# Optimization experiments

Hardware: AMD Instinct MI355X
Metric: run time of the kernel (lower is better)

Reference implementation:

```python
import jax, jax.numpy as jnp
import numpy as np

LEAKY_SLOPE = 0.01  # torch nn.LeakyReLU default

def _mlp(x, w1, b1, w2, b2):
    # MLP_Layer(num_layers=2, batch_norm=False): Linear -> ReLU -> Linear
    return jax.nn.relu(x @ w1 + b1) @ w2 + b2

def _edge_softmax(scores, dst, num_nodes):
    # softmax over incoming edges of each destination node; scores: [E, H]
    m = jax.ops.segment_max(scores, dst, num_segments=num_nodes)  # [N, H]
    e = jnp.exp(scores - m[dst])
    s = jax.ops.segment_sum(e, dst, num_segments=num_nodes)       # [N, H]
    return e / s[dst]

def setup_inputs() -> dict:
    key = jax.random.key(0)
    ks = jax.random.split(key, 10)
    N, E, H = 50000, 800000, 4
    D_H, PCA, PI, HID = 64, 64, 32, 128
    inp = {
        "h":    jax.random.normal(ks[0], (N, D_H), jnp.float32),
        "pca":  jax.random.normal(ks[1], (N, PCA), jnp.float32),
        "pimg": jax.random.normal(ks[2], (N, PI), jnp.float32),
        "pca_w1": jax.random.normal(ks[3], (2 * PCA, HID), jnp.float32) * (1.0 / np.sqrt(2 * PCA)),
        "pca_b1": jnp.zeros((HID,), jnp.float32),
        "pca_w2": jax.random.normal(ks[4], (HID, H), jnp.float32) * (1.0 / np.sqrt(HID)),
        "pca_b2": jnp.zeros((H,), jnp.float32),
        "pi_w1": jax.random.normal(ks[5], (2 * PI, HID), jnp.float32) * (1.0 / np.sqrt(2 * PI)),
        "pi_b1": jnp.zeros((HID,), jnp.float32),
        "pi_w2": jax.random.normal(ks[6], (HID, H), jnp.float32) * (1.0 / np.sqrt(HID)),
        "pi_b2": jnp.zeros((H,), jnp.float32),
        "src": jax.random.randint(ks[7], (E,), 0, N, jnp.int32),
        "dst": jax.random.randint(ks[8], (E,), 0, N, jnp.int32),
    }
    return inp

def reference(h, pca, pimg, pca_w1, pca_b1, pca_w2, pca_b2,
              pi_w1, pi_b1, pi_w2, pi_b2, src, dst):
    N = h.shape[0]

    def attend(feat, w1, b1, w2, b2):
        e_feat = jnp.concatenate([feat[src], feat[dst]], axis=1)        # [E, 2F]
        score = jax.nn.leaky_relu(_mlp(e_feat, w1, b1, w2, b2), LEAKY_SLOPE)  # [E, H]
        a = _edge_softmax(score, dst, N)                                # [E, H]
        msg = h[src][:, None, :] * a[:, :, None]                        # [E, H, D]
        return jax.ops.segment_sum(msg, dst, num_segments=N)           # [N, H, D]

    out_pca = attend(pca, pca_w1, pca_b1, pca_w2, pca_b2)
    out_pi = attend(pimg, pi_w1, pi_b1, pi_w2, pi_b2)
    return jnp.concatenate([out_pca, out_pi], axis=-1)                  # [N, H, 2D]
```

## Files before the change

kernel.cpp:

```cpp
#include <hip/hip_runtime.h>
#include <hip/hip_fp16.h>

constexpr int HID = 128;
constexpr int DH  = 64;

typedef _Float16 f16x2 __attribute__((ext_vector_type(2)));
typedef _Float16 fh4   __attribute__((ext_vector_type(4)));
typedef _Float16 fh8   __attribute__((ext_vector_type(8)));
typedef float    f32x4v __attribute__((ext_vector_type(4)));

__device__ __forceinline__ fh8 relu8(fh8 x) {
  fh8 z = {0, 0, 0, 0, 0, 0, 0, 0};
#if __has_builtin(__builtin_elementwise_max)
  return __builtin_elementwise_max(x, z);
#else
  fh8 r;
#pragma unroll
  for (int i = 0; i < 8; i++) r[i] = x[i] > z[i] ? x[i] : z[i];
  return r;
#endif
}

__global__ void count_h16_kernel(const int* __restrict__ dst, int* __restrict__ counts, int E,
                                 const float* __restrict__ h, _Float16* __restrict__ h16, int total) {
  int i = blockIdx.x * 256 + threadIdx.x;
  if (i < E) atomicAdd(&counts[dst[i]], 1);
  int base = i * 8;
  if (base + 7 < total) {
    float4 f0 = *(const float4*)(h + base);
    float4 f1 = *(const float4*)(h + base + 4);
    fh8 t;
    t[0] = (_Float16)f0.x; t[1] = (_Float16)f0.y; t[2] = (_Float16)f0.z; t[3] = (_Float16)f0.w;
    t[4] = (_Float16)f1.x; t[5] = (_Float16)f1.y; t[6] = (_Float16)f1.z; t[7] = (_Float16)f1.w;
    *(fh8*)(h16 + base) = t;
  }
}

__launch_bounds__(256)
__global__ void uv_mfma_kernel(const float* __restrict__ pca, const float* __restrict__ pimg,
                               const float* __restrict__ b1a, const float* __restrict__ b1b,
                               const float* __restrict__ w1a, const float* __restrict__ w1b,
                               _Float16* __restrict__ u_cat, _Float16* __restrict__ v_cat, int N) {
  __shared__ _Float16 sB[16384];
  int rel = blockIdx.y;
  const float* feat = rel ? pimg : pca;
  const float* b1   = rel ? b1b : b1a;
  const float* w1   = rel ? w1b : w1a;
  int F  = rel ? 32 : 64;
  int KS = rel ? 1 : 2;
  int tid = threadIdx.x;
  for (int idx = tid; idx < 16384; idx += 256) {
    int g = idx >> 10, s = (idx >> 9) & 1, l = (idx >> 3) & 63, j = idx & 7;
    int bc = l & 15, bkg = l >> 4;
    int k = s * 32 + bkg * 8 + j;
    float val = 0.f;
    if (k < F) {
      int jslot = (g & 7) * 16 + bc;
      int krow = (g < 8) ? k : (F + k);
      val = w1[krow * HID + jslot];
    }
    sB[idx] = (_Float16)val;
  }
  __syncthreads();
  int lane = tid & 63, w = tid >> 6;
  int c = lane & 15, kg = lane >> 4;
  int node = blockIdx.x * 64 + w * 16 + c;
  int nclamp = node < N ? node : N - 1;
  fh8 bfeat[2];
#pragma unroll
  for (int s = 0; s < 2; s++) {
    if (s < KS) {
      const float* fp = feat + (size_t)nclamp * F + s * 32 + kg * 8;
      float4 f0 = *(const float4*)fp;
      float4 f1 = *(const float4*)(fp + 4);
      fh8 t;
      t[0] = (_Float16)f0.x; t[1] = (_Float16)f0.y; t[2] = (_Float16)f0.z; t[3] = (_Float16)f0.w;
      t[4] = (_Float16)f1.x; t[5] = (_Float16)f1.y; t[6] = (_Float16)f1.z; t[7] = (_Float16)f1.w;
      bfeat[s] = t;
    }
  }
  float4 b1q[8];
#pragma unroll
  for (int g = 0; g < 8; g++) b1q[g] = *(const float4*)(b1 + g * 16 + kg * 4);

  bool wr = node < N;
#pragma unroll
  for (int g = 0; g < 16; g++) {
    f32x4v acc = {0.f, 0.f, 0.f, 0.f};
    acc = __builtin_amdgcn_mfma_f32_16x16x32_f16(((const fh8*)sB)[(g * 2 + 0) * 64 + lane], bfeat[0], acc, 0, 0, 0);
    if (KS == 2)
      acc = __builtin_amdgcn_mfma_f32_16x16x32_f16(((const fh8*)sB)[(g * 2 + 1) * 64 + lane], bfeat[1], acc, 0, 0, 0);
    bool isv = g >= 8;
    int jbase = (g & 7) * 16 + kg * 4;
    float4 bias = isv ? b1q[g & 7] : make_float4(0.f, 0.f, 0.f, 0.f);
    fh4 pk;
    pk[0] = (_Float16)(acc[0] + bias.x);
    pk[1] = (_Float16)(acc[1] + bias.y);
    pk[2] = (_Float16)(acc[2] + bias.z);
    pk[3] = (_Float16)(acc[3] + bias.w);
    _Float16* outp = isv ? v_cat : u_cat;
    if (wr) *(fh4*)(outp + (size_t)node * 256 + rel * 128 + jbase) = pk;
  }
}

__launch_bounds__(256)
__global__ void scan1_kernel(const int* __restrict__ counts, int* __restrict__ bsums, int N) {
  int b = blockIdx.x, tid = threadIdx.x;
  int base = b * 1024 + tid * 4;
  int s = 0;
  if (base + 3 < N) {
    int4 v = *(const int4*)(counts + base);
    s = v.x + v.y + v.z + v.w;
  } else {
    for (int q = 0; q < 4; q++) { int idx = base + q; if (idx < N) s += counts[idx]; }
  }
#pragma unroll
  for (int o = 32; o >= 1; o >>= 1) s += __shfl_xor(s, o);
  __shared__ int ws[4];
  if ((tid & 63) == 0) ws[tid >> 6] = s;
  __syncthreads();
  if (tid == 0) bsums[b] = ws[0] + ws[1] + ws[2] + ws[3];
}

__launch_bounds__(256)
__global__ void scan23_kernel(const int* __restrict__ counts, const int* __restrict__ bsums,
                              int* __restrict__ offsets, int* __restrict__ cursor,
                              int NB, int N, int E) {
  int b = blockIdx.x, tid = threadIdx.x, lane = tid & 63, w = tid >> 6;
  __shared__ int s_bpre;
  if (tid < 64) {
    int v = (lane < NB) ? bsums[lane] : 0;
    int incl = v;
#pragma unroll
    for (int o = 1; o < 64; o <<= 1) { int t = __shfl_up(incl, o); if (lane >= o) incl += t; }
    int excl = incl - v;
    int t = __shfl(excl, b);
    if (lane == 0) s_bpre = t;
  }
  __syncthreads();
  int base = b * 1024 + tid * 4;
  int c[4] = {0, 0, 0, 0};
  if (base + 3 < N) {
    int4 v = *(const int4*)(counts + base);
    c[0] = v.x; c[1] = v.y; c[2] = v.z; c[3] = v.w;
  } else {
    for (int q = 0; q < 4; q++) { int idx = base + q; if (idx < N) c[q] = counts[idx]; }
  }
  int s = c[0] + c[1] + c[2] + c[3];
  int incl = s;
#pragma unroll
  for (int o = 1; o < 64; o <<= 1) { int t = __shfl_up(incl, o); if (lane >= o) incl += t; }
  int excl = incl - s;
  __shared__ int ws[4];
  if (lane == 63) ws[w] = incl;
  __syncthreads();
  int wpre = 0;
  for (int q = 0; q < w; q++) wpre += ws[q];
  int off = s_bpre + wpre + excl;
  for (int q = 0; q < 4; q++) {
    int idx = base + q;
    if (idx < N) { offsets[idx] = off; cursor[idx] = off; }
    off += c[q];
  }
  if (b == 0 && tid == 0) offsets[N] = E;
}

__global__ void fill_kernel(const int* __restrict__ src, const int* __restrict__ dst,
                            int* __restrict__ cursor, int2* __restrict__ edges, int E) {
  int e = blockIdx.x * 256 + threadIdx.x;
  if (e < E) {
    int d = dst[e];
    int pos = atomicAdd(&cursor[d], 1);
    edges[pos] = make_int2(src[e], d);
  }
}

__launch_bounds__(256, 8)
__global__ void score_kernel(const _Float16* __restrict__ u_cat, const _Float16* __restrict__ v_cat,
                             const int2* __restrict__ edges,
                             const float* __restrict__ w2a, const float* __restrict__ w2b,
                             const float* __restrict__ b2a, const float* __restrict__ b2b,
                             _Float16* __restrict__ ek, int E) {
  __shared__ _Float16 sB[8 * 64 * 8];
  int tid = threadIdx.x, lane = tid & 63, w = tid >> 6;
  int col = lane & 15, kg = lane >> 4;
  for (int idx = tid; idx < 4096; idx += 256) {
    int t = idx >> 9, l = (idx >> 3) & 63, j = idx & 7;
    int bc = l & 15;
    int k = t * 32 + ((l >> 4) << 3) + j;
    float val = 0.f;
    if (bc < 4) { if (k < 128) val = w2a[k * 4 + bc]; }
    else if (bc < 8) { if (k >= 128) val = w2b[(k - 128) * 4 + (bc - 4)]; }
    sB[idx] = (_Float16)val;
  }
  __syncthreads();

  int ebase = blockIdx.x * 256 + w * 64;
  const _Float16* up[4];
  const _Float16* vp[4];
#pragma unroll
  for (int m = 0; m < 4; m++) {
    int em = ebase + m * 16 + col;
    int ec = em < E ? em : 0;
    int2 sd = edges[ec];
    up[m] = u_cat + (size_t)sd.x * 256 + kg * 8;
    vp[m] = v_cat + (size_t)sd.y * 256 + kg * 8;
  }

  f32x4v acc[4];
#pragma unroll
  for (int m = 0; m < 4; m++) acc[m] = (f32x4v){0.f, 0.f, 0.f, 0.f};

#pragma unroll
  for (int t = 0; t < 8; t++) {
    fh8 bf = *(const fh8*)(sB + ((t * 64 + lane) << 3));
#pragma unroll
    for (int m = 0; m < 4; m++) {
      fh8 uu = *(const fh8*)(up[m] + t * 32);
      fh8 vv = *(const fh8*)(vp[m] + t * 32);
      acc[m] = __builtin_amdgcn_mfma_f32_16x16x32_f16(relu8(uu + vv), bf, acc[m], 0, 0, 0);
    }
  }

  if (col < 8) {
    float b2v = (col < 4) ? b2a[col] : b2b[col - 4];
#pragma unroll
    for (int m = 0; m < 4; m++) {
#pragma unroll
      for (int q = 0; q < 4; q++) {
        int er = ebase + m * 16 + kg * 4 + q;
        if (er < E) {
          float x = acc[m][q] + b2v;
          x = x > 0.f ? x : 0.01f * x;
          ek[(size_t)er * 8 + col] = (_Float16)__expf(x);
        }
      }
    }
  }
}

__launch_bounds__(256, 8)
__global__ void agg_kernel(const _Float16* __restrict__ ek, const int2* __restrict__ edges,
                           const int* __restrict__ offsets, const _Float16* __restrict__ h16,
                           float* __restrict__ out, int N) {
  int wid = blockIdx.x * 4 + (threadIdx.x >> 6);
  int lane = threadIdx.x & 63;
  if (wid >= N) return;
  int off0 = offsets[wid], off1 = offsets[wid + 1];
  int deg = off1 - off0;
  float* op = out + (size_t)wid * 512;
  if (deg == 0) {
#pragma unroll
    for (int k = 0; k < 4; k++) { op[k * 128 + lane] = 0.f; op[k * 128 + 64 + lane] = 0.f; }
    return;
  }
  float accO[8] = {0, 0, 0, 0, 0, 0, 0, 0};
  float ssum[8] = {0, 0, 0, 0, 0, 0, 0, 0};
  int last = off1 - 1;
  int s0 = edges[off0].x;
  int s1 = edges[min(off0 + 1, last)].x;
  int s2 = edges[min(off0 + 2, last)].x;
  int s3 = edges[min(off0 + 3, last)].x;
  for (int jj = 0; jj < deg; jj += 4) {
    int i0 = off0 + jj;
    int i1 = min(i0 + 1, last), i2 = min(i0 + 2, last), i3 = min(i0 + 3, last);
    bool m1 = jj + 1 < deg, m2 = jj + 2 < deg, m3 = jj + 3 < deg;
    fh8 e0 = *(const fh8*)(ek + (size_t)i0 * 8);
    fh8 e1 = *(const fh8*)(ek + (size_t)i1 * 8);
    fh8 e2 = *(const fh8*)(ek + (size_t)i2 * 8);
    fh8 e3 = *(const fh8*)(ek + (size_t)i3 * 8);
    float hv0 = (float)h16[(size_t)s0 * DH + lane];
    float hv1 = (float)h16[(size_t)s1 * DH + lane];
    float hv2 = (float)h16[(size_t)s2 * DH + lane];
    float hv3 = (float)h16[(size_t)s3 * DH + lane];
    int t0 = edges[min(i0 + 4, last)].x;
    int t1 = edges[min(i0 + 5, last)].x;
    int t2 = edges[min(i0 + 6, last)].x;
    int t3 = edges[min(i0 + 7, last)].x;
#pragma unroll
    for (int k = 0; k < 8; k++) {
      float e0v = (float)e0[k];
      float e1v = m1 ? (float)e1[k] : 0.f;
      float e2v = m2 ? (float)e2[k] : 0.f;
      float e3v = m3 ? (float)e3[k] : 0.f;
      accO[k] = fmaf(e0v, hv0, accO[k]);
      accO[k] = fmaf(e1v, hv1, accO[k]);
      accO[k] = fmaf(e2v, hv2, accO[k]);
      accO[k] = fmaf(e3v, hv3, accO[k]);
      ssum[k] += (e0v + e1v) + (e2v + e3v);
    }
    s0 = t0; s1 = t1; s2 = t2; s3 = t3;
  }
#pragma unroll
  for (int k = 0; k < 8; k++) {
    float rsv = 1.f / ssum[k];
    int colo = k < 4 ? k * 128 + lane : (k - 4) * 128 + 64 + lane;
    op[colo] = accO[k] * rsv;
  }
}

extern "C" void kernel_launch(void* const* d_in, const int* in_sizes, int n_in,
                              void* d_out, int out_size, void* d_ws, size_t ws_size,
                              hipStream_t stream) {
  const float* h      = (const float*)d_in[0];
  const float* pca    = (const float*)d_in[1];
  const float* pimg   = (const float*)d_in[2];
  const float* pca_w1 = (const float*)d_in[3];
  const float* pca_b1 = (const float*)d_in[4];
  const float* pca_w2 = (const float*)d_in[5];
  const float* pca_b2 = (const float*)d_in[6];
  const float* pi_w1  = (const float*)d_in[7];
  const float* pi_b1  = (const float*)d_in[8];
  const float* pi_w2  = (const float*)d_in[9];
  const float* pi_b2  = (const float*)d_in[10];
  const int*   src    = (const int*)d_in[11];
  const int*   dst    = (const int*)d_in[12];
  int N = in_sizes[0] / 64;
  int E = in_sizes[11];
  float* out = (float*)d_out;

  char* ws = (char*)d_ws;
  size_t o = 0;
  auto alloc = [&](size_t bytes) { void* p = ws + o; o += (bytes + 255) & ~(size_t)255; return p; };
  _Float16* u_cat  = (_Float16*)alloc((size_t)N * 256 * 2);
  _Float16* v_cat  = (_Float16*)alloc((size_t)N * 256 * 2);
  _Float16* h16    = (_Float16*)alloc((size_t)N * 64 * 2);
  int* counts  = (int*)alloc((size_t)N * 4);
  int* cursor  = (int*)alloc((size_t)N * 4);
  int* offsets = (int*)alloc((size_t)(N + 1) * 4);
  int* bsums   = (int*)alloc(1024 * 4);
  int2* edges  = (int2*)alloc((size_t)E * 8);
  _Float16* ekb = (_Float16*)alloc((size_t)E * 8 * 2);

  hipMemsetAsync(counts, 0, (size_t)N * 4, stream);

  count_h16_kernel<<<(E + 255) / 256, 256, 0, stream>>>(dst, counts, E, h, h16, N * 64);
  dim3 uvgrid((N + 63) / 64, 2);
  uv_mfma_kernel<<<uvgrid, 256, 0, stream>>>(pca, pimg, pca_b1, pi_b1, pca_w1, pi_w1, u_cat, v_cat, N);
  int NB = (N + 1023) / 1024;
  scan1_kernel<<<NB, 256, 0, stream>>>(counts, bsums, N);
  scan23_kernel<<<NB, 256, 0, stream>>>(counts, bsums, offsets, cursor, NB, N, E);
  fill_kernel<<<(E + 255) / 256, 256, 0, stream>>>(src, dst, cursor, edges, E);
  score_kernel<<<(E + 255) / 256, 256, 0, stream>>>(u_cat, v_cat, edges,
                                                    pca_w2, pi_w2, pca_b2, pi_b2, ekb, E);
  agg_kernel<<<(N + 3) / 4, 256, 0, stream>>>(ekb, edges, offsets, h16, out, N);
}
```

Before: 304.8 us.

## Fuse edge scoring with CSR aggregation and precompute W1 fragment table once

The separate score and aggregation kernels are merged. Each wave takes a 64-edge chunk of the dst-sorted edge list, finds its node range by binary search over the offsets, computes the exp scores with MFMA into shared memory, and then accumulates h-weighted messages per destination node, writing each output row when it reaches a node boundary. This removes the round trip of the E×8 fp16 score buffer through global memory and one kernel launch. The W1 fragment layout is also built once into a global table by the count kernel, so the uv blocks copy it instead of rebuilding it from scattered fp32 loads. In exchange, the aggregation loop now runs serially per edge with no unrolling, occupancy is lowered to 6 blocks, and waves do uneven work because of binary search and boundary handling.

```diff
diff --git a/kernel.cpp b/kernel.cpp
--- a/kernel.cpp
+++ b/kernel.cpp
@@ -21,9 +21,28 @@
 #endif
 }
 
-__global__ void count_h16_kernel(const int* __restrict__ dst, int* __restrict__ counts, int E,
-                                 const float* __restrict__ h, _Float16* __restrict__ h16, int total) {
+__global__ void count_h16_frag_kernel(const int* __restrict__ dst, int* __restrict__ counts, int E,
+                                      const float* __restrict__ h, _Float16* __restrict__ h16, int total,
+                                      const float* __restrict__ w1a, const float* __restrict__ w1b,
+                                      _Float16* __restrict__ fragTab) {
   int i = blockIdx.x * 256 + threadIdx.x;
+  if (blockIdx.x < 128) {
+    int flat = i;
+    int rel = flat >> 14;
+    int r2 = flat & 16383;
+    int g = r2 >> 10, s = (r2 >> 9) & 1, l = (r2 >> 3) & 63, j = r2 & 7;
+    int bc = l & 15, bkg = l >> 4;
+    int k = s * 32 + bkg * 8 + j;
+    int F = rel ? 32 : 64;
+    const float* w1 = rel ? w1b : w1a;
+    float val = 0.f;
+    if (k < F) {
+      int jslot = (g & 7) * 16 + bc;
+      int krow = (g < 8) ? k : (F + k);
+      val = w1[krow * HID + jslot];
+    }
+    fragTab[flat] = (_Float16)val;
+  }
   if (i < E) atomicAdd(&counts[dst[i]], 1);
   int base = i * 8;
   if (base + 7 < total) {
@@ -39,27 +58,19 @@
 __launch_bounds__(256)
 __global__ void uv_mfma_kernel(const float* __restrict__ pca, const float* __restrict__ pimg,
                                const float* __restrict__ b1a, const float* __restrict__ b1b,
-                               const float* __restrict__ w1a, const float* __restrict__ w1b,
+                               const _Float16* __restrict__ fragTab,
                                _Float16* __restrict__ u_cat, _Float16* __restrict__ v_cat, int N) {
   __shared__ _Float16 sB[16384];
   int rel = blockIdx.y;
   const float* feat = rel ? pimg : pca;
   const float* b1   = rel ? b1b : b1a;
-  const float* w1   = rel ? w1b : w1a;
   int F  = rel ? 32 : 64;
   int KS = rel ? 1 : 2;
   int tid = threadIdx.x;
-  for (int idx = tid; idx < 16384; idx += 256) {
-    int g = idx >> 10, s = (idx >> 9) & 1, l = (idx >> 3) & 63, j = idx & 7;
-    int bc = l & 15, bkg = l >> 4;
-    int k = s * 32 + bkg * 8 + j;
-    float val = 0.f;
-    if (k < F) {
-      int jslot = (g & 7) * 16 + bc;
-      int krow = (g < 8) ? k : (F + k);
-      val = w1[krow * HID + jslot];
-    }
-    sB[idx] = (_Float16)val;
+  {
+    const fh8* srcp = (const fh8*)(fragTab + rel * 16384);
+    fh8* dstp = (fh8*)sB;
+    for (int i = tid; i < 2048; i += 256) dstp[i] = srcp[i];
   }
   __syncthreads();
   int lane = tid & 63, w = tid >> 6;
@@ -175,14 +186,17 @@
   }
 }
 
-__launch_bounds__(256, 8)
-__global__ void score_kernel(const _Float16* __restrict__ u_cat, const _Float16* __restrict__ v_cat,
-                             const int2* __restrict__ edges,
+__launch_bounds__(256, 6)
+__global__ void fused_kernel(const _Float16* __restrict__ u_cat, const _Float16* __restrict__ v_cat,
+                             const int2* __restrict__ edges, const int* __restrict__ offsets,
+                             const _Float16* __restrict__ h16,
                              const float* __restrict__ w2a, const float* __restrict__ w2b,
                              const float* __restrict__ b2a, const float* __restrict__ b2b,
-                             _Float16* __restrict__ ek, int E) {
-  __shared__ _Float16 sB[8 * 64 * 8];
-  int tid = threadIdx.x, lane = tid & 63, w = tid >> 6;
+                             float* __restrict__ out, int N, int NW) {
+  __shared__ _Float16 sB[4096];
+  __shared__ __align__(16) _Float16 s_ek[4][64][8];
+  __shared__ int s_src[4][64];
+  int tid = threadIdx.x, lane = tid & 63, wv = tid >> 6;
   int col = lane & 15, kg = lane >> 4;
   for (int idx = tid; idx < 4096; idx += 256) {
     int t = idx >> 9, l = (idx >> 3) & 63, j = idx & 7;
@@ -195,107 +209,121 @@
   }
   __syncthreads();
 
-  int ebase = blockIdx.x * 256 + w * 64;
-  const _Float16* up[4];
-  const _Float16* vp[4];
-#pragma unroll
-  for (int m = 0; m < 4; m++) {
-    int em = ebase + m * 16 + col;
-    int ec = em < E ? em : 0;
-    int2 sd = edges[ec];
-    up[m] = u_cat + (size_t)sd.x * 256 + kg * 8;
-    vp[m] = v_cat + (size_t)sd.y * 256 + kg * 8;
-  }
-
-  f32x4v acc[4];
-#pragma unroll
-  for (int m = 0; m < 4; m++) acc[m] = (f32x4v){0.f, 0.f, 0.f, 0.f};
-
-#pragma unroll
-  for (int t = 0; t < 8; t++) {
-    fh8 bf = *(const fh8*)(sB + ((t * 64 + lane) << 3));
+  int w = blockIdx.x * 4 + wv;
+  if (w >= NW) return;
+  int t0 = w * 64, t1 = t0 + 64;
+  int lo = 0, hi = N;
+  while (lo < hi) { int mid = (lo + hi) >> 1; if (offsets[mid] < t0) lo = mid + 1; else hi = mid; }
+  int nlo = lo;
+  hi = N;
+  while (lo < hi) { int mid = (lo + hi) >> 1; if (offsets[mid] < t1) lo = mid + 1; else hi = mid; }
+  int nhi = lo;
+  if (nlo >= nhi) return;
+  int e_begin = offsets[nlo], e_end = offsets[nhi];
+
+  float b2v = (col < 4) ? b2a[col] : ((col < 8) ? b2b[col - 4] : 0.f);
+
+  int cur = nlo;
+  int node_start = e_begin;
+  int boundary = offsets[cur + 1];
+  float accO[8] = {0, 0, 0, 0, 0, 0, 0, 0};
+  float ssum[8] = {0, 0, 0, 0, 0, 0, 0, 0};
+
+  for (int cb = e_begin; cb < e_end; cb += 64) {
+    __builtin_amdgcn_wave_barrier();
+    const _Float16* up[4];
+    const _Float16* vp[4];
+    int srcs[4];
 #pragma unroll
     for (int m = 0; m < 4; m++) {
-      fh8 uu = *(const fh8*)(up[m] + t * 32);
-      fh8 vv = *(const fh8*)(vp[m] + t * 32);
-      acc[m] = __builtin_amdgcn_mfma_f32_16x16x32_f16(relu8(uu + vv), bf, acc[m], 0, 0, 0);
-    }
-  }
-
-  if (col < 8) {
-    float b2v = (col < 4) ? b2a[col] : b2b[col - 4];
-#pragma unroll
-    for (int m = 0; m < 4; m++) {
-#pragma unroll
-      for (int q = 0; q < 4; q++) {
-        int er = ebase + m * 16 + kg * 4 + q;
-        if (er < E) {
+      int em = cb + m * 16 + col;
+      int ec = em < e_end ? em : e_end - 1;
+      int2 sd = edges[ec];
+      srcs[m] = sd.x;
+      up[m] = u_cat + (size_t)sd.x * 256 + kg * 8;
+      vp[m] = v_cat + (size_t)sd.y * 256 + kg * 8;
+    }
+    f32x4v acc[4];
+#pragma unroll
+    for (int m = 0; m < 4; m++) acc[m] = (f32x4v){0.f, 0.f, 0.f, 0.f};
+#pragma unroll
+    for (int t = 0; t < 8; t++) {
+      fh8 bf = *(const fh8*)(sB + ((t * 64 + lane) << 3));
+#pragma unroll
+      for (int m = 0; m < 4; m++) {
+        fh8 uu = *(const fh8*)(up[m] + t * 32);
+        fh8 vv = *(const fh8*)(vp[m] + t * 32);
+        acc[m] = __builtin_amdgcn_mfma_f32_16x16x32_f16(relu8(uu + vv), bf, acc[m], 0, 0, 0);
+      }
+    }
+    if (kg == 0) {
+#pragma unroll
+      for (int m = 0; m < 4; m++) s_src[wv][m * 16 + col] = srcs[m];
+    }
+    if (col < 8) {
+#pragma unroll
+      for (int m = 0; m < 4; m++) {
+#pragma unroll
+        for (int q = 0; q < 4; q++) {
           float x = acc[m][q] + b2v;
           x = x > 0.f ? x : 0.01f * x;
-          ek[(size_t)er * 8 + col] = (_Float16)__expf(x);
+          s_ek[wv][m * 16 + kg * 4 + q][col] = (_Float16)__expf(x);
         }
       }
     }
-  }
-}
-
-__launch_bounds__(256, 8)
-__global__ void agg_kernel(const _Float16* __restrict__ ek, const int2* __restrict__ edges,
-                           const int* __restrict__ offsets, const _Float16* __restrict__ h16,
-                           float* __restrict__ out, int N) {
-  int wid = blockIdx.x * 4 + (threadIdx.x >> 6);
-  int lane = threadIdx.x & 63;
-  if (wid >= N) return;
-  int off0 = offsets[wid], off1 = offsets[wid + 1];
-  int deg = off1 - off0;
-  float* op = out + (size_t)wid * 512;
-  if (deg == 0) {
-#pragma unroll
-    for (int k = 0; k < 4; k++) { op[k * 128 + lane] = 0.f; op[k * 128 + 64 + lane] = 0.f; }
-    return;
-  }
-  float accO[8] = {0, 0, 0, 0, 0, 0, 0, 0};
-  float ssum[8] = {0, 0, 0, 0, 0, 0, 0, 0};
-  int last = off1 - 1;
-  int s0 = edges[off0].x;
-  int s1 = edges[min(off0 + 1, last)].x;
-  int s2 = edges[min(off0 + 2, last)].x;
-  int s3 = edges[min(off0 + 3, last)].x;
-  for (int jj = 0; jj < deg; jj += 4) {
-    int i0 = off0 + jj;
-    int i1 = min(i0 + 1, last), i2 = min(i0 + 2, last), i3 = min(i0 + 3, last);
-    bool m1 = jj + 1 < deg, m2 = jj + 2 < deg, m3 = jj + 3 < deg;
-    fh8 e0 = *(const fh8*)(ek + (size_t)i0 * 8);
-    fh8 e1 = *(const fh8*)(ek + (size_t)i1 * 8);
-    fh8 e2 = *(const fh8*)(ek + (size_t)i2 * 8);
-    fh8 e3 = *(const fh8*)(ek + (size_t)i3 * 8);
-    float hv0 = (float)h16[(size_t)s0 * DH + lane];
-    float hv1 = (float)h16[(size_t)s1 * DH + lane];
-    float hv2 = (float)h16[(size_t)s2 * DH + lane];
-    float hv3 = (float)h16[(size_t)s3 * DH + lane];
-    int t0 = edges[min(i0 + 4, last)].x;
-    int t1 = edges[min(i0 + 5, last)].x;
-    int t2 = edges[min(i0 + 6, last)].x;
-    int t3 = edges[min(i0 + 7, last)].x;
-#pragma unroll
-    for (int k = 0; k < 8; k++) {
-      float e0v = (float)e0[k];
-      float e1v = m1 ? (float)e1[k] : 0.f;
-      float e2v = m2 ? (float)e2[k] : 0.f;
-      float e3v = m3 ? (float)e3[k] : 0.f;
-      accO[k] = fmaf(e0v, hv0, accO[k]);
-      accO[k] = fmaf(e1v, hv1, accO[k]);
-      accO[k] = fmaf(e2v, hv2, accO[k]);
-      accO[k] = fmaf(e3v, hv3, accO[k]);
-      ssum[k] += (e0v + e1v) + (e2v + e3v);
-    }
-    s0 = t0; s1 = t1; s2 = t2; s3 = t3;
-  }
-#pragma unroll
-  for (int k = 0; k < 8; k++) {
-    float rsv = 1.f / ssum[k];
-    int colo = k < 4 ? k * 128 + lane : (k - 4) * 128 + 64 + lane;
-    op[colo] = accO[k] * rsv;
+    __builtin_amdgcn_wave_barrier();
+    asm volatile("s_waitcnt lgkmcnt(0)" ::: "memory");
+    int cnt = min(64, e_end - cb);
+    for (int jj = 0; jj < cnt; jj++) {
+      int e = cb + jj;
+      while (e == boundary) {
+        int deg = boundary - node_start;
+        float* op = out + (size_t)cur * 512;
+        if (deg == 0) {
+#pragma unroll
+          for (int k = 0; k < 4; k++) { op[k * 128 + lane] = 0.f; op[k * 128 + 64 + lane] = 0.f; }
+        } else {
+#pragma unroll
+          for (int k = 0; k < 8; k++) {
+            float rsv = 1.f / ssum[k];
+            int colo = k < 4 ? k * 128 + lane : (k - 4) * 128 + 64 + lane;
+            op[colo] = accO[k] * rsv;
+          }
+        }
+#pragma unroll
+        for (int k = 0; k < 8; k++) { accO[k] = 0.f; ssum[k] = 0.f; }
+        node_start = boundary; cur++;
+        boundary = offsets[cur + 1];
+      }
+      fh8 ea = *(const fh8*)(&s_ek[wv][jj][0]);
+      int sa = s_src[wv][jj];
+      float hv = (float)h16[(size_t)sa * DH + lane];
+#pragma unroll
+      for (int k = 0; k < 8; k++) {
+        float ev = (float)ea[k];
+        accO[k] = fmaf(ev, hv, accO[k]);
+        ssum[k] += ev;
+      }
+    }
+  }
+  while (cur < nhi) {
+    int bnd = offsets[cur + 1];
+    int deg = bnd - node_start;
+    float* op = out + (size_t)cur * 512;
+    if (deg == 0) {
+#pragma unroll
+      for (int k = 0; k < 4; k++) { op[k * 128 + lane] = 0.f; op[k * 128 + 64 + lane] = 0.f; }
+    } else {
+#pragma unroll
+      for (int k = 0; k < 8; k++) {
+        float rsv = 1.f / ssum[k];
+        int colo = k < 4 ? k * 128 + lane : (k - 4) * 128 + 64 + lane;
+        op[colo] = accO[k] * rsv;
+      }
+    }
+#pragma unroll
+    for (int k = 0; k < 8; k++) { accO[k] = 0.f; ssum[k] = 0.f; }
+    node_start = bnd; cur++;
   }
 }
 
@@ -325,23 +353,24 @@
   _Float16* u_cat  = (_Float16*)alloc((size_t)N * 256 * 2);
   _Float16* v_cat  = (_Float16*)alloc((size_t)N * 256 * 2);
   _Float16* h16    = (_Float16*)alloc((size_t)N * 64 * 2);
+  _Float16* fragTab = (_Float16*)alloc(32768 * 2);
   int* counts  = (int*)alloc((size_t)N * 4);
   int* cursor  = (int*)alloc((size_t)N * 4);
   int* offsets = (int*)alloc((size_t)(N + 1) * 4);
   int* bsums   = (int*)alloc(1024 * 4);
   int2* edges  = (int2*)alloc((size_t)E * 8);
-  _Float16* ekb = (_Float16*)alloc((size_t)E * 8 * 2);
 
   hipMemsetAsync(counts, 0, (size_t)N * 4, stream);
 
-  count_h16_kernel<<<(E + 255) / 256, 256, 0, stream>>>(dst, counts, E, h, h16, N * 64);
+  count_h16_frag_kernel<<<(E + 255) / 256, 256, 0, stream>>>(dst, counts, E, h, h16, N * 64,
+                                                             pca_w1, pi_w1, fragTab);
   dim3 uvgrid((N + 63) / 64, 2);
-  uv_mfma_kernel<<<uvgrid, 256, 0, stream>>>(pca, pimg, pca_b1, pi_b1, pca_w1, pi_w1, u_cat, v_cat, N);
+  uv_mfma_kernel<<<uvgrid, 256, 0, stream>>>(pca, pimg, pca_b1, pi_b1, fragTab, u_cat, v_cat, N);
   int NB = (N + 1023) / 1024;
   scan1_kernel<<<NB, 256, 0, stream>>>(counts, bsums, N);
   scan23_kernel<<<NB, 256, 0, stream>>>(counts, bsums, offsets, cursor, NB, N, E);
   fill_kernel<<<(E + 255) / 256, 256, 0, stream>>>(src, dst, cursor, edges, E);
-  score_kernel<<<(E + 255) / 256, 256, 0, stream>>>(u_cat, v_cat, edges,
-                                                    pca_w2, pi_w2, pca_b2, pi_b2, ekb, E);
-  agg_kernel<<<(N + 3) / 4, 256, 0, stream>>>(ekb, edges, offsets, h16, out, N);
-}
+  int NW = (E + 63) / 64;
+  fused_kernel<<<(NW + 3) / 4, 256, 0, stream>>>(u_cat, v_cat, edges, offsets, h16,
+                                                 pca_w2, pi_w2, pca_b2, pi_b2, out, N, NW);
+}
```

Result: slower. 332.6 us (+9.1%).
